# Kernel tuning notes

Measured on AMD Instinct MI355X. Metric: run time of the kernel, lower is better.

The kernel has to match this reference:

```python
import jax, jax.numpy as jnp
from jax import lax
import numpy as np

B, S, H, NF, K, POOL = 64, 1024, 256, 256, 7, 3  # batch, seq, encoded, num_filters, kernel_size, max_pool
C = NF  # input channels must equal num_filters for the per-sample conv


def setup_inputs() -> dict:
    key = jax.random.key(0)
    ks = jax.random.split(key, 8)
    s = lambda k, shape, sc=0.05: jax.random.normal(k, shape, jnp.float32) * sc
    return dict(
        x=jax.random.normal(ks[0], (B, S, C), jnp.float32),
        layer=1,
        gru_kernel_f=s(ks[1], (C, 3 * H)),
        gru_rec_f=s(ks[2], (H, 3 * H)),
        gru_bias_f=jnp.zeros((2, 3 * H), jnp.float32),
        gru_kernel_b=s(ks[3], (C, 3 * H)),
        gru_rec_b=s(ks[4], (H, 3 * H)),
        gru_bias_b=jnp.zeros((2, 3 * H), jnp.float32),
        Wa=s(ks[5], (2 * H, NF * H)),      # hyper_a: Dense(encoded*num_filters), no bias
        Wb=s(ks[6], (H, K * NF)),          # hyper_b: Dense(kernel_size*num_filters), no bias
        conv_bias=jnp.zeros((NF,), jnp.float32),
    )


def _gru_last(x, Wk, Wr, b):
    """Keras GRU (reset_after=True), return final hidden state. x: [B,S,C]."""
    xp = jnp.einsum('bsc,ch->bsh', x, Wk) + b[0]  # precompute input projections
    h0 = jnp.zeros((x.shape[0], Wr.shape[0]), x.dtype)

    def step(h, xt):
        hp = h @ Wr + b[1]
        xz, xr, xh = jnp.split(xt, 3, axis=-1)
        hz, hr, hn = jnp.split(hp, 3, axis=-1)
        z = jax.nn.sigmoid(xz + hz)
        r = jax.nn.sigmoid(xr + hr)
        hh = jnp.tanh(xh + r * hn)
        return z * h + (1.0 - z) * hh, None

    hT, _ = lax.scan(step, h0, jnp.swapaxes(xp, 0, 1))
    return hT


def reference(x, layer, gru_kernel_f, gru_rec_f, gru_bias_f, gru_kernel_b, gru_rec_b,
              gru_bias_b, Wa, Wb, conv_bias):
    if layer == 0:
        pad = (NF - x.shape[2]) // 2
        x = jnp.pad(x, ((0, 0), (0, 0), (pad, pad)))
    # Bidirectional GRU output (return_sequences=False): concat of final fwd/bwd states
    hf = _gru_last(x, gru_kernel_f, gru_rec_f, gru_bias_f)
    hb = _gru_last(x[:, ::-1], gru_kernel_b, gru_rec_b, gru_bias_b)
    c = jnp.concatenate([hf, hb], axis=-1)  # [B, 2H]
    # Hypernetwork: per-sample conv filters
    a = (c @ Wa).reshape(B, NF, H)                          # filters_a: [B, NF, H]
    fb = jnp.einsum('bne,ef->bnf', a, Wb).reshape(B, NF, NF, K)
    filt = fb.transpose(0, 3, 2, 1)                         # [B, K, C_in, C_out] (tf.transpose reversal)

    def conv1(xi, fi):  # xi [S,C], fi [K,C,C]
        return lax.conv_general_dilated(xi[None], fi, (1,), 'SAME',
                                        dimension_numbers=('NWC', 'WIO', 'NWC'))[0]

    y = jax.vmap(conv1)(x, filt) + conv_bias                # [B, S, NF]
    y = jax.nn.relu(y)
    # MaxPooling1D(pool_size=3), stride 3, VALID
    L = (y.shape[1] // POOL) * POOL
    return y[:, :L].reshape(B, L // POOL, POOL, NF).max(axis=2)
```

## Files before the change

kernel.cpp:

```cpp
#include <hip/hip_runtime.h>
#include <cstddef>

typedef unsigned int  uint;
typedef unsigned short ushort_t;
typedef __attribute__((ext_vector_type(8))) short bf16x8;
typedef __attribute__((ext_vector_type(4))) float f32x4;
typedef __attribute__((ext_vector_type(2))) _Float16 h2_t;

__device__ __forceinline__ short f2bs(float x) {
    union { float f; uint u; } v; v.f = x;
    uint r = v.u + 0x7FFF + ((v.u >> 16) & 1);
    return (short)(r >> 16);
}
__device__ __forceinline__ ushort_t f16b(float x) {
    _Float16 h = (_Float16)x; return __builtin_bit_cast(ushort_t, h);
}
__device__ __forceinline__ float h2f(ushort_t u) {
    return (float)__builtin_bit_cast(_Float16, u);
}
__device__ __forceinline__ float fdot2a(uint a, uint b, float c) {
#if __has_builtin(__builtin_amdgcn_fdot2)
    return __builtin_amdgcn_fdot2(__builtin_bit_cast(h2_t, a), __builtin_bit_cast(h2_t, b), c, false);
#else
    h2_t ha = __builtin_bit_cast(h2_t, a), hb = __builtin_bit_cast(h2_t, b);
    return c + (float)ha.x * (float)hb.x + (float)ha.y * (float)hb.y;
#endif
}
__device__ __forceinline__ float fast_sigmoid(float x) {
    float e = __builtin_amdgcn_exp2f(-1.4426950408889634f * x);
    return __builtin_amdgcn_rcpf(1.f + e);
}
__device__ __forceinline__ float fast_tanh(float x) {
    float e = __builtin_amdgcn_exp2f(2.8853900817779268f * x);
    return 1.f - 2.f * __builtin_amdgcn_rcpf(e + 1.f);
}

#define MFMA16(a,b,c) __builtin_amdgcn_mfma_f32_16x16x32_bf16((a),(b),(c),0,0,0)

__global__ void k_prep_x(const float* __restrict__ x, short* __restrict__ xb) {
    int i = (blockIdx.x * 256 + threadIdx.x) * 4;
    float4 v = *(const float4*)&x[i];
    short o[4] = { f2bs(v.x), f2bs(v.y), f2bs(v.z), f2bs(v.w) };
    *(uint2*)&xb[i] = *(uint2*)o;
}
__global__ void k_prep_wk(const float* __restrict__ kf, const float* __restrict__ kb,
                          short* __restrict__ wkt) {
    int n = blockIdx.x, k = threadIdx.x;
    float v = (n < 768) ? kf[k * 768 + n] : kb[k * 768 + (n - 768)];
    wkt[n * 256 + k] = f2bs(v);
}
__global__ void k_prep_wr(const float* __restrict__ wrf, const float* __restrict__ wrb,
                          uint4* __restrict__ wp) {
    int idx = blockIdx.x * 256 + threadIdx.x;
    int dir = idx / 24576, rem = idx % 24576;
    int g = rem / 8192, rem2 = rem % 8192;
    int kc = rem2 / 256, j = rem2 % 256;
    int col = g * 256 + j;
    const float* w = dir ? wrb : wrf;
    uint c[4];
#pragma unroll
    for (int d = 0; d < 4; d++) {
        int k0 = kc * 8 + d * 2;
        uint lo = f16b(w[k0 * 768 + col]);
        uint hi = f16b(w[(k0 + 1) * 768 + col]);
        c[d] = lo | (hi << 16);
    }
    wp[idx] = make_uint4(c[0], c[1], c[2], c[3]);
}
__global__ void k_prep_wb(const float* __restrict__ wb, short* __restrict__ wbt) {
    int kp = blockIdx.x, e = threadIdx.x;
    int n2 = kp & 255, kk = kp >> 8;
    int f = n2 * 7 + kk;
    wbt[kp * 256 + e] = f2bs(wb[e * 1792 + f]);
}

__global__ __launch_bounds__(512) void k_proj(const short* __restrict__ xb,
        const short* __restrict__ wkt, const float* __restrict__ gbf,
        const float* __restrict__ gbb, ushort_t* __restrict__ xp) {
    __shared__ union {
        struct { short A[128 * 40]; short B[128 * 40]; } st;
        ushort_t E[128 * 136];
    } u;
    int bid = blockIdx.x;
    int nt = bid % 12, mt = bid / 12;
    int r0 = mt * 128, n0 = nt * 128;
    int tid = threadIdx.x, lane = tid & 63, wid = tid >> 6;
    int wm = wid & 1, wn = wid >> 1;
    int q = lane >> 4, c = lane & 15;
    f32x4 acc[4][2];
#pragma unroll
    for (int mi = 0; mi < 4; mi++)
#pragma unroll
        for (int ni = 0; ni < 2; ni++) acc[mi][ni] = (f32x4){0.f, 0.f, 0.f, 0.f};
    int si = tid >> 2, sp = tid & 3;
    for (int kt = 0; kt < 8; kt++) {
        int k0 = kt * 32;
        *(uint4*)&u.st.A[si * 40 + sp * 8] = *(const uint4*)&xb[(r0 + si) * 256 + k0 + sp * 8];
        *(uint4*)&u.st.B[si * 40 + sp * 8] = *(const uint4*)&wkt[(n0 + si) * 256 + k0 + sp * 8];
        __syncthreads();
        bf16x8 af[4], bfr[2];
#pragma unroll
        for (int mi = 0; mi < 4; mi++) af[mi] = *(bf16x8*)&u.st.A[(wm * 64 + mi * 16 + c) * 40 + q * 8];
#pragma unroll
        for (int ni = 0; ni < 2; ni++) bfr[ni] = *(bf16x8*)&u.st.B[(wn * 32 + ni * 16 + c) * 40 + q * 8];
#pragma unroll
        for (int mi = 0; mi < 4; mi++)
#pragma unroll
            for (int ni = 0; ni < 2; ni++) acc[mi][ni] = MFMA16(af[mi], bfr[ni], acc[mi][ni]);
        __syncthreads();
    }
#pragma unroll
    for (int ni = 0; ni < 2; ni++) {
        int ng = n0 + wn * 32 + ni * 16 + c;
        bool d1 = ng >= 768; int nb = d1 ? ng - 768 : ng;
        float bias = d1 ? gbb[nb] : gbf[nb];
#pragma unroll
        for (int mi = 0; mi < 4; mi++)
#pragma unroll
            for (int v = 0; v < 4; v++) {
                int rl = wm * 64 + mi * 16 + q * 4 + v;
                u.E[rl * 136 + wn * 32 + ni * 16 + c] = f16b(acc[mi][ni][v] + bias);
            }
    }
    __syncthreads();
    {
        int i = tid >> 2, p = tid & 3;
        int r = r0 + i, b = r >> 10, t = r & 1023;
        int ng = n0 + p * 32;
        const ushort_t* src = &u.E[i * 136 + p * 32];
        ushort_t* dst;
        if (ng < 768) dst = xp + (size_t)(b * 1024 + t) * 768 + ng;
        else          dst = xp + 50331648ull + (size_t)(b * 1024 + (1023 - t)) * 768 + (ng - 768);
#pragma unroll
        for (int v = 0; v < 4; v++) *(uint4*)&dst[v * 8] = *(const uint4*)&src[v * 8];
    }
}

__global__ __launch_bounds__(512, 2) void k_gru(const uint4* __restrict__ wp,
        const ushort_t* __restrict__ xp, const float* __restrict__ gbf,
        const float* __restrict__ gbb, float* __restrict__ cbuf) {
    int wg = blockIdx.x;
    int dir = wg >> 6, b = wg & 63;
    int tid = threadIdx.x;
    int lane = tid & 63, w = tid >> 6;
    int half = lane >> 5;
    int j = w * 32 + (lane & 31);
    const uint4* W = wp + dir * 24576 + half * 4096 + j;
    uint4 wz[16], wr[16], wn[16];
#pragma unroll
    for (int kc = 0; kc < 16; kc++) {
        wz[kc] = W[kc * 256];
        wr[kc] = W[8192 + kc * 256];
        wn[kc] = W[16384 + kc * 256];
    }
    __shared__ uint4 hbuf[2][32];
    const float* bs = (dir ? gbb : gbf) + 768 + j;
    float bz = bs[0], br = bs[256], bn = bs[512];
    const ushort_t* X = xp + ((size_t)dir * 64 + b) * 786432 + j;
    ushort_t uz = X[0], ur = X[256], un = X[512];
    const ushort_t* Xn = X + 768;
    float h = 0.f;
    if (tid < 32) hbuf[0][tid] = (uint4){0, 0, 0, 0};
    __syncthreads();
#pragma unroll 1
    for (int tt = 0; tt < 1024; tt++) {
        const uint4* hb = &hbuf[tt & 1][half * 16];
        ushort_t nz = Xn[0], nr = Xn[256], nn = Xn[512];
        Xn += 768;
        float az = 0.f, ar = 0.f, an = 0.f;
        uint4 c0 = hb[0], c1 = hb[1], c2 = hb[2], c3 = hb[3];
#pragma unroll
        for (int ch = 0; ch < 4; ch++) {
            uint4 n0, n1, n2, n3;
            if (ch < 3) {
                n0 = hb[ch * 4 + 4]; n1 = hb[ch * 4 + 5];
                n2 = hb[ch * 4 + 6]; n3 = hb[ch * 4 + 7];
            }
            int kb = ch * 4;
#define DOT1(hc, kk)                                                              \
            az = fdot2a(hc.x, wz[kk].x, az); ar = fdot2a(hc.x, wr[kk].x, ar);     \
            an = fdot2a(hc.x, wn[kk].x, an);                                      \
            az = fdot2a(hc.y, wz[kk].y, az); ar = fdot2a(hc.y, wr[kk].y, ar);     \
            an = fdot2a(hc.y, wn[kk].y, an);                                      \
            az = fdot2a(hc.z, wz[kk].z, az); ar = fdot2a(hc.z, wr[kk].z, ar);     \
            an = fdot2a(hc.z, wn[kk].z, an);                                      \
            az = fdot2a(hc.w, wz[kk].w, az); ar = fdot2a(hc.w, wr[kk].w, ar);     \
            an = fdot2a(hc.w, wn[kk].w, an);
            DOT1(c0, kb + 0) DOT1(c1, kb + 1) DOT1(c2, kb + 2) DOT1(c3, kb + 3)
#undef DOT1
            __builtin_amdgcn_sched_barrier(0);
            if (ch < 3) { c0 = n0; c1 = n1; c2 = n2; c3 = n3; }
        }
        az += __shfl_xor(az, 32, 64);
        ar += __shfl_xor(ar, 32, 64);
        an += __shfl_xor(an, 32, 64);
        float z = fast_sigmoid(h2f(uz) + az + bz);
        float r = fast_sigmoid(h2f(ur) + ar + br);
        float hh = fast_tanh(h2f(un) + r * (an + bn));
        h = z * h + (1.f - z) * hh;
        uz = nz; ur = nr; un = nn;
        if (half == 0) ((ushort_t*)&hbuf[(tt & 1) ^ 1][0])[j] = f16b(h);
        __syncthreads();
    }
    if (half == 0) cbuf[b * 512 + dir * 256 + j] = h;
}

__global__ __launch_bounds__(256) void k_hyper1(const float* __restrict__ cbuf,
        const float* __restrict__ Wa, short* __restrict__ aout) {
    __shared__ union {
        struct { short A[64 * 40]; short B[128 * 40]; } st;
        ushort_t E[64 * 136];
    } u;
    int nt = blockIdx.x, n0 = nt * 128;
    int tid = threadIdx.x, lane = tid & 63, wid = tid >> 6;
    int q = lane >> 4, c = lane & 15;
    f32x4 acc[4][2];
#pragma unroll
    for (int mi = 0; mi < 4; mi++)
#pragma unroll
        for (int ni = 0; ni < 2; ni++) acc[mi][ni] = (f32x4){0.f, 0.f, 0.f, 0.f};
    for (int kt = 0; kt < 16; kt++) {
        int k0 = kt * 32;
        {
            int i = tid >> 2, p = tid & 3;
            const float* s = &cbuf[i * 512 + k0 + p * 8];
            short tmp[8];
#pragma unroll
            for (int v = 0; v < 8; v++) tmp[v] = f2bs(s[v]);
            *(uint4*)&u.st.A[i * 40 + p * 8] = *(uint4*)tmp;
        }
        {
            int kk = tid >> 3, nn0 = (tid & 7) * 16;
            const float* s = &Wa[(size_t)(k0 + kk) * 65536 + n0 + nn0];
#pragma unroll
            for (int l = 0; l < 16; l++) u.st.B[(nn0 + l) * 40 + kk] = f2bs(s[l]);
        }
        __syncthreads();
        bf16x8 af[4], bfr[2];
#pragma unroll
        for (int mi = 0; mi < 4; mi++) af[mi] = *(bf16x8*)&u.st.A[(mi * 16 + c) * 40 + q * 8];
#pragma unroll
        for (int ni = 0; ni < 2; ni++) bfr[ni] = *(bf16x8*)&u.st.B[(wid * 32 + ni * 16 + c) * 40 + q * 8];
#pragma unroll
        for (int mi = 0; mi < 4; mi++)
#pragma unroll
            for (int ni = 0; ni < 2; ni++) acc[mi][ni] = MFMA16(af[mi], bfr[ni], acc[mi][ni]);
        __syncthreads();
    }
#pragma unroll
    for (int ni = 0; ni < 2; ni++)
#pragma unroll
        for (int mi = 0; mi < 4; mi++)
#pragma unroll
            for (int v = 0; v < 4; v++)
                u.E[(mi * 16 + q * 4 + v) * 136 + wid * 32 + ni * 16 + c] =
                    (ushort_t)f2bs(acc[mi][ni][v]);
    __syncthreads();
    {
        int i = tid >> 2, p = tid & 3;
        short* dst = aout + (size_t)i * 65536 + n0 + p * 32;
        const ushort_t* src = &u.E[i * 136 + p * 32];
#pragma unroll
        for (int v = 0; v < 4; v++) *(uint4*)&dst[v * 8] = *(const uint4*)&src[v * 8];
    }
}

__global__ __launch_bounds__(512) void k_hyper2(const short* __restrict__ a,
        const short* __restrict__ wbt, short* __restrict__ wc) {
    __shared__ union {
        struct { short A[128 * 40]; short B[128 * 40]; } st;
        ushort_t E[128 * 136];
    } u;
    int bid = blockIdx.x;
    int nt = bid % 14, mt = bid / 14;
    int r0 = mt * 128, n0 = nt * 128;
    int tid = threadIdx.x, lane = tid & 63, wid = tid >> 6;
    int wm = wid & 1, wn = wid >> 1;
    int q = lane >> 4, c = lane & 15;
    f32x4 acc[4][2];
#pragma unroll
    for (int mi = 0; mi < 4; mi++)
#pragma unroll
        for (int ni = 0; ni < 2; ni++) acc[mi][ni] = (f32x4){0.f, 0.f, 0.f, 0.f};
    int si = tid >> 2, sp = tid & 3;
    for (int kt = 0; kt < 8; kt++) {
        int k0 = kt * 32;
        *(uint4*)&u.st.A[si * 40 + sp * 8] = *(const uint4*)&a[(r0 + si) * 256 + k0 + sp * 8];
        *(uint4*)&u.st.B[si * 40 + sp * 8] = *(const uint4*)&wbt[(n0 + si) * 256 + k0 + sp * 8];
        __syncthreads();
        bf16x8 af[4], bfr[2];
#pragma unroll
        for (int mi = 0; mi < 4; mi++) af[mi] = *(bf16x8*)&u.st.A[(wm * 64 + mi * 16 + c) * 40 + q * 8];
#pragma unroll
        for (int ni = 0; ni < 2; ni++) bfr[ni] = *(bf16x8*)&u.st.B[(wn * 32 + ni * 16 + c) * 40 + q * 8];
#pragma unroll
        for (int mi = 0; mi < 4; mi++)
#pragma unroll
            for (int ni = 0; ni < 2; ni++) acc[mi][ni] = MFMA16(af[mi], bfr[ni], acc[mi][ni]);
        __syncthreads();
    }
#pragma unroll
    for (int ni = 0; ni < 2; ni++)
#pragma unroll
        for (int mi = 0; mi < 4; mi++)
#pragma unroll
            for (int v = 0; v < 4; v++)
                u.E[(wm * 64 + mi * 16 + q * 4 + v) * 136 + wn * 32 + ni * 16 + c] =
                    (ushort_t)f2bs(acc[mi][ni][v]);
    __syncthreads();
    {
        int i = tid >> 2, p = tid & 3;
        int r = r0 + i, b = r >> 8, co = r & 255;
        short* dst = wc + (size_t)(b * 256 + co) * 1792 + n0 + p * 32;
        const ushort_t* src = &u.E[i * 136 + p * 32];
#pragma unroll
        for (int v = 0; v < 4; v++) *(uint4*)&dst[v * 8] = *(const uint4*)&src[v * 8];
    }
}

__global__ __launch_bounds__(512) void k_conv(const short* __restrict__ xb,
        const short* __restrict__ wc, const float* __restrict__ cbias,
        float* __restrict__ out) {
    __shared__ union {
        struct { short A[128 * 72]; short B[256 * 72]; } st;
        ushort_t Y[128 * 256];
    } u;
    int bid = blockIdx.x;
    int bb = bid & 63, mt = bid >> 6;
    int s0 = mt * 126, p0 = mt * 42;
    int tid = threadIdx.x, lane = tid & 63, wid = tid >> 6;
    int wm = wid & 1, wn = wid >> 1;
    int q = lane >> 4, c = lane & 15;
    const short* xbb = xb + (size_t)bb * 262144;
    const short* wcb = wc + (size_t)bb * 458752;
    f32x4 acc[4][4];
#pragma unroll
    for (int mi = 0; mi < 4; mi++)
#pragma unroll
        for (int ni = 0; ni < 4; ni++) acc[mi][ni] = (f32x4){0.f, 0.f, 0.f, 0.f};
    for (int kc = 0; kc < 28; kc++) {
        int k = kc >> 2, c0 = (kc & 3) * 64;
        {
            int i = tid >> 2, p = tid & 3;
            int rs = s0 + i + k - 3;
            uint4 v0 = {0, 0, 0, 0}, v1 = {0, 0, 0, 0};
            if (rs >= 0 && rs < 1024) {
                const uint4* s = (const uint4*)&xbb[rs * 256 + c0 + p * 16];
                v0 = s[0]; v1 = s[1];
            }
            uint4* d = (uint4*)&u.st.A[i * 72 + p * 16];
            d[0] = v0; d[1] = v1;
        }
        {
            int co = tid >> 1, p = tid & 1;
            const uint4* s = (const uint4*)&wcb[co * 1792 + kc * 64 + p * 32];
            uint4* d = (uint4*)&u.st.B[co * 72 + p * 32];
            d[0] = s[0]; d[1] = s[1]; d[2] = s[2]; d[3] = s[3];
        }
        __syncthreads();
        bf16x8 af[4][2], bfr[4][2];
#pragma unroll
        for (int mi = 0; mi < 4; mi++)
#pragma unroll
            for (int kt = 0; kt < 2; kt++)
                af[mi][kt] = *(bf16x8*)&u.st.A[(wm * 64 + mi * 16 + c) * 72 + kt * 32 + q * 8];
#pragma unroll
        for (int ni = 0; ni < 4; ni++)
#pragma unroll
            for (int kt = 0; kt < 2; kt++)
                bfr[ni][kt] = *(bf16x8*)&u.st.B[(wn * 64 + ni * 16 + c) * 72 + kt * 32 + q * 8];
#pragma unroll
        for (int kt = 0; kt < 2; kt++)
#pragma unroll
            for (int mi = 0; mi < 4; mi++)
#pragma unroll
                for (int ni = 0; ni < 4; ni++)
                    acc[mi][ni] = MFMA16(af[mi][kt], bfr[ni][kt], acc[mi][ni]);
        __syncthreads();
    }
#pragma unroll
    for (int ni = 0; ni < 4; ni++) {
        int cg = wn * 64 + ni * 16 + c;
        float bias = cbias[cg];
#pragma unroll
        for (int mi = 0; mi < 4; mi++)
#pragma unroll
            for (int v = 0; v < 4; v++) {
                int rl = wm * 64 + mi * 16 + q * 4 + v;
                float val = acc[mi][ni][v] + bias;
                u.Y[rl * 256 + cg] = f16b(fmaxf(val, 0.f));
            }
    }
    __syncthreads();
    for (int it = 0; it < 21; it++) {
        int idx = it * 512 + tid;
        int pp = idx >> 8, co = idx & 255;
        int p = p0 + pp;
        if (p < 341) {
            float a0 = h2f(u.Y[(3 * pp) * 256 + co]);
            float a1 = h2f(u.Y[(3 * pp + 1) * 256 + co]);
            float a2 = h2f(u.Y[(3 * pp + 2) * 256 + co]);
            out[(size_t)(bb * 341 + p) * 256 + co] = fmaxf(fmaxf(a0, a1), a2);
        }
    }
}

extern "C" void kernel_launch(void* const* d_in, const int* in_sizes, int n_in,
                              void* d_out, int out_size, void* d_ws, size_t ws_size,
                              hipStream_t stream) {
    const float* x    = (const float*)d_in[0];
    const float* gkf  = (const float*)d_in[2];
    const float* grf  = (const float*)d_in[3];
    const float* gbf  = (const float*)d_in[4];
    const float* gkb  = (const float*)d_in[5];
    const float* grb  = (const float*)d_in[6];
    const float* gbb  = (const float*)d_in[7];
    const float* Wa   = (const float*)d_in[8];
    const float* Wb   = (const float*)d_in[9];
    const float* cbias= (const float*)d_in[10];
    float* out = (float*)d_out;
    char* ws = (char*)d_ws;

    short*    xb   = (short*)(ws);
    ushort_t* xp   = (ushort_t*)(ws + 33554432);
    short*    wkt  = (short*)(ws + 234881024);
    uint4*    wp   = (uint4*)(ws + 235667456);
    short*    wbt  = (short*)(ws + 236453888);
    float*    cbuf = (float*)(ws + 237371392);
    short*    aout = (short*)(ws + 237502464);
    short*    wc   = (short*)(ws + 245891072);

    hipLaunchKernelGGL(k_prep_x,  dim3(16384), dim3(256), 0, stream, x, xb);
    hipLaunchKernelGGL(k_prep_wk, dim3(1536),  dim3(256), 0, stream, gkf, gkb, wkt);
    hipLaunchKernelGGL(k_prep_wr, dim3(192),   dim3(256), 0, stream, grf, grb, wp);
    hipLaunchKernelGGL(k_prep_wb, dim3(1792),  dim3(256), 0, stream, Wb, wbt);
    hipLaunchKernelGGL(k_proj,    dim3(6144),  dim3(512), 0, stream, xb, wkt, gbf, gbb, xp);
    hipLaunchKernelGGL(k_gru,     dim3(128),   dim3(512), 0, stream, wp, xp, gbf, gbb, cbuf);
    hipLaunchKernelGGL(k_hyper1,  dim3(512),   dim3(256), 0, stream, cbuf, Wa, aout);
    hipLaunchKernelGGL(k_hyper2,  dim3(1792),  dim3(512), 0, stream, aout, wbt, wc);
    hipLaunchKernelGGL(k_conv,    dim3(576),   dim3(512), 0, stream, xb, wc, cbias, out);
}
```

Measured before the change: 1.570 ms.

## Repartition GRU recurrent matvec: two columns per lane, K split four ways

The recurrent GRU kernel now has each lane compute two adjacent output columns over a quarter of the hidden dimension, instead of one column over half. Weights are repacked into a per-k-pair uint layout, and hidden-state LDS reads use a rotated per-quarter offset to avoid bank conflicts. Partial sums are reduced with two shuffle stages. The aim is fewer LDS reads of h per FMA and better dot-product throughput on the serial critical path, at the cost of extra shuffles and select logic.

```diff
diff --git a/kernel.cpp b/kernel.cpp
--- a/kernel.cpp
+++ b/kernel.cpp
@@ -50,22 +50,18 @@
     wkt[n * 256 + k] = f2bs(v);
 }
 __global__ void k_prep_wr(const float* __restrict__ wrf, const float* __restrict__ wrb,
-                          uint4* __restrict__ wp) {
+                          uint* __restrict__ wp2) {
     int idx = blockIdx.x * 256 + threadIdx.x;
-    int dir = idx / 24576, rem = idx % 24576;
-    int g = rem / 8192, rem2 = rem % 8192;
-    int kc = rem2 / 256, j = rem2 % 256;
+    int j = idx & 255;
+    int rest = idx >> 8;
+    int p = rest & 127;
+    int gg = rest >> 7;
+    int g = gg % 3, dir = gg / 3;
+    const float* w = dir ? wrb : wrf;
     int col = g * 256 + j;
-    const float* w = dir ? wrb : wrf;
-    uint c[4];
-#pragma unroll
-    for (int d = 0; d < 4; d++) {
-        int k0 = kc * 8 + d * 2;
-        uint lo = f16b(w[k0 * 768 + col]);
-        uint hi = f16b(w[(k0 + 1) * 768 + col]);
-        c[d] = lo | (hi << 16);
-    }
-    wp[idx] = make_uint4(c[0], c[1], c[2], c[3]);
+    uint lo = f16b(w[(2 * p) * 768 + col]);
+    uint hi = f16b(w[(2 * p + 1) * 768 + col]);
+    wp2[idx] = lo | (hi << 16);
 }
 __global__ void k_prep_wb(const float* __restrict__ wb, short* __restrict__ wbt) {
     int kp = blockIdx.x, e = threadIdx.x;
@@ -136,73 +132,109 @@
     }
 }
 
-__global__ __launch_bounds__(512, 2) void k_gru(const uint4* __restrict__ wp,
+__global__ __launch_bounds__(512, 2) void k_gru(const uint* __restrict__ wp2,
         const ushort_t* __restrict__ xp, const float* __restrict__ gbf,
         const float* __restrict__ gbb, float* __restrict__ cbuf) {
     int wg = blockIdx.x;
     int dir = wg >> 6, b = wg & 63;
     int tid = threadIdx.x;
     int lane = tid & 63, w = tid >> 6;
-    int half = lane >> 5;
-    int j = w * 32 + (lane & 31);
-    const uint4* W = wp + dir * 24576 + half * 4096 + j;
-    uint4 wz[16], wr[16], wn[16];
-#pragma unroll
-    for (int kc = 0; kc < 16; kc++) {
-        wz[kc] = W[kc * 256];
-        wr[kc] = W[8192 + kc * 256];
-        wn[kc] = W[16384 + kc * 256];
-    }
-    __shared__ uint4 hbuf[2][32];
-    const float* bs = (dir ? gbb : gbf) + 768 + j;
+    int jl = lane & 15;
+    int kh = (lane >> 4) & 3;
+    int hi = lane >> 5;
+    int j0 = w * 32 + jl * 2;
+    int jsel = j0 + hi;
+
+    const uint* WB = wp2 + dir * 98304;
+    uint2 wreg[3][8][4];
+#pragma unroll
+    for (int g = 0; g < 3; g++)
+#pragma unroll
+        for (int i = 0; i < 8; i++)
+#pragma unroll
+            for (int d = 0; d < 4; d++) {
+                int p = kh * 32 + ((i + kh) & 7) * 4 + d;
+                wreg[g][i][d] = *(const uint2*)&WB[(g * 128 + p) * 256 + j0];
+            }
+
+    __shared__ __align__(16) uint hb[2][128];
+    const float* bs = (dir ? gbb : gbf) + 768 + jsel;
     float bz = bs[0], br = bs[256], bn = bs[512];
-    const ushort_t* X = xp + ((size_t)dir * 64 + b) * 786432 + j;
+    const ushort_t* X = xp + ((size_t)dir * 64 + b) * 786432 + jsel;
     ushort_t uz = X[0], ur = X[256], un = X[512];
     const ushort_t* Xn = X + 768;
     float h = 0.f;
-    if (tid < 32) hbuf[0][tid] = (uint4){0, 0, 0, 0};
+    if (tid < 128) hb[0][tid] = 0u;
     __syncthreads();
+
+    const int off0 = kh * 128 + (((0 + kh) & 7) << 4);
+    const int off1 = kh * 128 + (((1 + kh) & 7) << 4);
+    const int off2 = kh * 128 + (((2 + kh) & 7) << 4);
+    const int off3 = kh * 128 + (((3 + kh) & 7) << 4);
+    const int off4 = kh * 128 + (((4 + kh) & 7) << 4);
+    const int off5 = kh * 128 + (((5 + kh) & 7) << 4);
+    const int off6 = kh * 128 + (((6 + kh) & 7) << 4);
+    const int off7 = kh * 128 + (((7 + kh) & 7) << 4);
+
+#define LDH(off) (*(const uint4*)((const char*)hbp + (off)))
+#define DOT8(cv, ii)                                                                     \
+    a00 = fdot2a(cv.x, wreg[0][ii][0].x, a00); a01 = fdot2a(cv.x, wreg[0][ii][0].y, a01);\
+    a10 = fdot2a(cv.x, wreg[1][ii][0].x, a10); a11 = fdot2a(cv.x, wreg[1][ii][0].y, a11);\
+    a20 = fdot2a(cv.x, wreg[2][ii][0].x, a20); a21 = fdot2a(cv.x, wreg[2][ii][0].y, a21);\
+    a00 = fdot2a(cv.y, wreg[0][ii][1].x, a00); a01 = fdot2a(cv.y, wreg[0][ii][1].y, a01);\
+    a10 = fdot2a(cv.y, wreg[1][ii][1].x, a10); a11 = fdot2a(cv.y, wreg[1][ii][1].y, a11);\
+    a20 = fdot2a(cv.y, wreg[2][ii][1].x, a20); a21 = fdot2a(cv.y, wreg[2][ii][1].y, a21);\
+    a00 = fdot2a(cv.z, wreg[0][ii][2].x, a00); a01 = fdot2a(cv.z, wreg[0][ii][2].y, a01);\
+    a10 = fdot2a(cv.z, wreg[1][ii][2].x, a10); a11 = fdot2a(cv.z, wreg[1][ii][2].y, a11);\
+    a20 = fdot2a(cv.z, wreg[2][ii][2].x, a20); a21 = fdot2a(cv.z, wreg[2][ii][2].y, a21);\
+    a00 = fdot2a(cv.w, wreg[0][ii][3].x, a00); a01 = fdot2a(cv.w, wreg[0][ii][3].y, a01);\
+    a10 = fdot2a(cv.w, wreg[1][ii][3].x, a10); a11 = fdot2a(cv.w, wreg[1][ii][3].y, a11);\
+    a20 = fdot2a(cv.w, wreg[2][ii][3].x, a20); a21 = fdot2a(cv.w, wreg[2][ii][3].y, a21);
+
 #pragma unroll 1
     for (int tt = 0; tt < 1024; tt++) {
-        const uint4* hb = &hbuf[tt & 1][half * 16];
+        const char* hbp = (const char*)&hb[tt & 1][0];
         ushort_t nz = Xn[0], nr = Xn[256], nn = Xn[512];
         Xn += 768;
-        float az = 0.f, ar = 0.f, an = 0.f;
-        uint4 c0 = hb[0], c1 = hb[1], c2 = hb[2], c3 = hb[3];
-#pragma unroll
-        for (int ch = 0; ch < 4; ch++) {
-            uint4 n0, n1, n2, n3;
-            if (ch < 3) {
-                n0 = hb[ch * 4 + 4]; n1 = hb[ch * 4 + 5];
-                n2 = hb[ch * 4 + 6]; n3 = hb[ch * 4 + 7];
-            }
-            int kb = ch * 4;
-#define DOT1(hc, kk)                                                              \
-            az = fdot2a(hc.x, wz[kk].x, az); ar = fdot2a(hc.x, wr[kk].x, ar);     \
-            an = fdot2a(hc.x, wn[kk].x, an);                                      \
-            az = fdot2a(hc.y, wz[kk].y, az); ar = fdot2a(hc.y, wr[kk].y, ar);     \
-            an = fdot2a(hc.y, wn[kk].y, an);                                      \
-            az = fdot2a(hc.z, wz[kk].z, az); ar = fdot2a(hc.z, wr[kk].z, ar);     \
-            an = fdot2a(hc.z, wn[kk].z, an);                                      \
-            az = fdot2a(hc.w, wz[kk].w, az); ar = fdot2a(hc.w, wr[kk].w, ar);     \
-            an = fdot2a(hc.w, wn[kk].w, an);
-            DOT1(c0, kb + 0) DOT1(c1, kb + 1) DOT1(c2, kb + 2) DOT1(c3, kb + 3)
-#undef DOT1
-            __builtin_amdgcn_sched_barrier(0);
-            if (ch < 3) { c0 = n0; c1 = n1; c2 = n2; c3 = n3; }
-        }
-        az += __shfl_xor(az, 32, 64);
-        ar += __shfl_xor(ar, 32, 64);
-        an += __shfl_xor(an, 32, 64);
-        float z = fast_sigmoid(h2f(uz) + az + bz);
-        float r = fast_sigmoid(h2f(ur) + ar + br);
-        float hh = fast_tanh(h2f(un) + r * (an + bn));
+        float a00 = 0.f, a01 = 0.f, a10 = 0.f, a11 = 0.f, a20 = 0.f, a21 = 0.f;
+        uint4 c0 = LDH(off0), c1 = LDH(off1);
+        uint4 n0 = LDH(off2), n1 = LDH(off3);
+        DOT8(c0, 0) DOT8(c1, 1)
+        __builtin_amdgcn_sched_barrier(0);
+        c0 = n0; c1 = n1;
+        n0 = LDH(off4); n1 = LDH(off5);
+        DOT8(c0, 2) DOT8(c1, 3)
+        __builtin_amdgcn_sched_barrier(0);
+        c0 = n0; c1 = n1;
+        n0 = LDH(off6); n1 = LDH(off7);
+        DOT8(c0, 4) DOT8(c1, 5)
+        __builtin_amdgcn_sched_barrier(0);
+        c0 = n0; c1 = n1;
+        DOT8(c0, 6) DOT8(c1, 7)
+
+        float s0, s1;
+        s0 = a00 + __shfl_xor(a00, 32, 64); s1 = a01 + __shfl_xor(a01, 32, 64);
+        float vz = hi ? s1 : s0;
+        s0 = a10 + __shfl_xor(a10, 32, 64); s1 = a11 + __shfl_xor(a11, 32, 64);
+        float vr = hi ? s1 : s0;
+        s0 = a20 + __shfl_xor(a20, 32, 64); s1 = a21 + __shfl_xor(a21, 32, 64);
+        float vn = hi ? s1 : s0;
+        vz += __shfl_xor(vz, 16, 64);
+        vr += __shfl_xor(vr, 16, 64);
+        vn += __shfl_xor(vn, 16, 64);
+
+        float z = fast_sigmoid(h2f(uz) + vz + bz);
+        float r = fast_sigmoid(h2f(ur) + vr + br);
+        float hh = fast_tanh(h2f(un) + r * (vn + bn));
         h = z * h + (1.f - z) * hh;
         uz = nz; ur = nr; un = nn;
-        if (half == 0) ((ushort_t*)&hbuf[(tt & 1) ^ 1][0])[j] = f16b(h);
-        __syncthreads();
-    }
-    if (half == 0) cbuf[b * 512 + dir * 256 + j] = h;
+        if (!(lane & 16))
+            ((ushort_t*)&hb[(tt & 1) ^ 1][0])[w * 32 + jl * 2 + hi] = f16b(h);
+        __syncthreads();
+    }
+#undef DOT8
+#undef LDH
+    if (!(lane & 16)) cbuf[b * 512 + dir * 256 + jsel] = h;
 }
 
 __global__ __launch_bounds__(256) void k_hyper1(const float* __restrict__ cbuf,
@@ -424,7 +456,7 @@
     short*    xb   = (short*)(ws);
     ushort_t* xp   = (ushort_t*)(ws + 33554432);
     short*    wkt  = (short*)(ws + 234881024);
-    uint4*    wp   = (uint4*)(ws + 235667456);
+    uint*     wp2  = (uint*)(ws + 235667456);
     short*    wbt  = (short*)(ws + 236453888);
     float*    cbuf = (float*)(ws + 237371392);
     short*    aout = (short*)(ws + 237502464);
@@ -432,10 +464,10 @@
 
     hipLaunchKernelGGL(k_prep_x,  dim3(16384), dim3(256), 0, stream, x, xb);
     hipLaunchKernelGGL(k_prep_wk, dim3(1536),  dim3(256), 0, stream, gkf, gkb, wkt);
-    hipLaunchKernelGGL(k_prep_wr, dim3(192),   dim3(256), 0, stream, grf, grb, wp);
+    hipLaunchKernelGGL(k_prep_wr, dim3(768),   dim3(256), 0, stream, grf, grb, wp2);
     hipLaunchKernelGGL(k_prep_wb, dim3(1792),  dim3(256), 0, stream, Wb, wbt);
     hipLaunchKernelGGL(k_proj,    dim3(6144),  dim3(512), 0, stream, xb, wkt, gbf, gbb, xp);
-    hipLaunchKernelGGL(k_gru,     dim3(128),   dim3(512), 0, stream, wp, xp, gbf, gbb, cbuf);
+    hipLaunchKernelGGL(k_gru,     dim3(128),   dim3(512), 0, stream, wp2, xp, gbf, gbb, cbuf);
     hipLaunchKernelGGL(k_hyper1,  dim3(512),   dim3(256), 0, stream, cbuf, Wa, aout);
     hipLaunchKernelGGL(k_hyper2,  dim3(1792),  dim3(512), 0, stream, aout, wbt, wc);
     hipLaunchKernelGGL(k_conv,    dim3(576),   dim3(512), 0, stream, xb, wc, cbias, out);
```

Measured after the change: 1.669 ms. +6.3%, slower.

## Batch GRU recurrence over 16 samples per block using f16 MFMA

Applied to the files above, without the earlier changes.

The recurrent GRU step now runs on fp16 MFMA instead of per-lane fdot2 dot products. Each block handles 16 batch samples of one direction, with the recurrent weights held in registers as MFMA B-fragments. The hidden state sits in a swizzled LDS buffer that serves as the A operand. This cuts the launch from 128 blocks to 8 and amortises the weight registers across samples, but uses only 8 CUs for the serial 1024-step loop and adds more per-step gate math per thread.

```diff
diff --git a/kernel.cpp b/kernel.cpp
--- a/kernel.cpp
+++ b/kernel.cpp
@@ -4,6 +4,7 @@
 typedef unsigned int  uint;
 typedef unsigned short ushort_t;
 typedef __attribute__((ext_vector_type(8))) short bf16x8;
+typedef __attribute__((ext_vector_type(8))) _Float16 f16x8;
 typedef __attribute__((ext_vector_type(4))) float f32x4;
 typedef __attribute__((ext_vector_type(2))) _Float16 h2_t;
 
@@ -18,14 +19,6 @@
 __device__ __forceinline__ float h2f(ushort_t u) {
     return (float)__builtin_bit_cast(_Float16, u);
 }
-__device__ __forceinline__ float fdot2a(uint a, uint b, float c) {
-#if __has_builtin(__builtin_amdgcn_fdot2)
-    return __builtin_amdgcn_fdot2(__builtin_bit_cast(h2_t, a), __builtin_bit_cast(h2_t, b), c, false);
-#else
-    h2_t ha = __builtin_bit_cast(h2_t, a), hb = __builtin_bit_cast(h2_t, b);
-    return c + (float)ha.x * (float)hb.x + (float)ha.y * (float)hb.y;
-#endif
-}
 __device__ __forceinline__ float fast_sigmoid(float x) {
     float e = __builtin_amdgcn_exp2f(-1.4426950408889634f * x);
     return __builtin_amdgcn_rcpf(1.f + e);
@@ -36,6 +29,7 @@
 }
 
 #define MFMA16(a,b,c) __builtin_amdgcn_mfma_f32_16x16x32_bf16((a),(b),(c),0,0,0)
+#define MFMAH(a,b,c)  __builtin_amdgcn_mfma_f32_16x16x32_f16((a),(b),(c),0,0,0)
 
 __global__ void k_prep_x(const float* __restrict__ x, short* __restrict__ xb) {
     int i = (blockIdx.x * 256 + threadIdx.x) * 4;
@@ -49,23 +43,11 @@
     float v = (n < 768) ? kf[k * 768 + n] : kb[k * 768 + (n - 768)];
     wkt[n * 256 + k] = f2bs(v);
 }
-__global__ void k_prep_wr(const float* __restrict__ wrf, const float* __restrict__ wrb,
-                          uint4* __restrict__ wp) {
-    int idx = blockIdx.x * 256 + threadIdx.x;
-    int dir = idx / 24576, rem = idx % 24576;
-    int g = rem / 8192, rem2 = rem % 8192;
-    int kc = rem2 / 256, j = rem2 % 256;
-    int col = g * 256 + j;
-    const float* w = dir ? wrb : wrf;
-    uint c[4];
-#pragma unroll
-    for (int d = 0; d < 4; d++) {
-        int k0 = kc * 8 + d * 2;
-        uint lo = f16b(w[k0 * 768 + col]);
-        uint hi = f16b(w[(k0 + 1) * 768 + col]);
-        c[d] = lo | (hi << 16);
-    }
-    wp[idx] = make_uint4(c[0], c[1], c[2], c[3]);
+__global__ void k_prep_wrt(const float* __restrict__ wrf, const float* __restrict__ wrb,
+                           ushort_t* __restrict__ wrt) {
+    int n = blockIdx.x, k = threadIdx.x;
+    float v = (n < 768) ? wrf[k * 768 + n] : wrb[k * 768 + (n - 768)];
+    wrt[n * 256 + k] = f16b(v);
 }
 __global__ void k_prep_wb(const float* __restrict__ wb, short* __restrict__ wbt) {
     int kp = blockIdx.x, e = threadIdx.x;
@@ -136,73 +118,104 @@
     }
 }
 
-__global__ __launch_bounds__(512, 2) void k_gru(const uint4* __restrict__ wp,
+__global__ __launch_bounds__(512, 2) void k_gru(const ushort_t* __restrict__ wrt,
         const ushort_t* __restrict__ xp, const float* __restrict__ gbf,
         const float* __restrict__ gbb, float* __restrict__ cbuf) {
-    int wg = blockIdx.x;
-    int dir = wg >> 6, b = wg & 63;
+    int g = blockIdx.x;
+    int dir = g >> 2;
     int tid = threadIdx.x;
     int lane = tid & 63, w = tid >> 6;
-    int half = lane >> 5;
-    int j = w * 32 + (lane & 31);
-    const uint4* W = wp + dir * 24576 + half * 4096 + j;
-    uint4 wz[16], wr[16], wn[16];
-#pragma unroll
-    for (int kc = 0; kc < 16; kc++) {
-        wz[kc] = W[kc * 256];
-        wr[kc] = W[8192 + kc * 256];
-        wn[kc] = W[16384 + kc * 256];
-    }
-    __shared__ uint4 hbuf[2][32];
-    const float* bs = (dir ? gbb : gbf) + 768 + j;
-    float bz = bs[0], br = bs[256], bn = bs[512];
-    const ushort_t* X = xp + ((size_t)dir * 64 + b) * 786432 + j;
-    ushort_t uz = X[0], ur = X[256], un = X[512];
-    const ushort_t* Xn = X + 768;
-    float h = 0.f;
-    if (tid < 32) hbuf[0][tid] = (uint4){0, 0, 0, 0};
+    int c = lane & 15, q = lane >> 4;
+    int bq = (g & 3) * 16 + q * 4;
+
+    const ushort_t* WD = wrt + (size_t)dir * 196608;
+    f16x8 wfr[6][8];
+#pragma unroll
+    for (int nt = 0; nt < 6; nt++) {
+        int gate = nt >> 1, sub = nt & 1;
+        const ushort_t* wp = WD + (size_t)(gate * 256 + w * 32 + sub * 16 + c) * 256 + q * 8;
+#pragma unroll
+        for (int kt = 0; kt < 8; kt++)
+            wfr[nt][kt] = *(const f16x8*)(wp + kt * 32);
+    }
+
+    const float* bsr = (dir ? gbb : gbf) + 768;
+    float bz[2], br[2], bn[2];
+#pragma unroll
+    for (int sub = 0; sub < 2; sub++) {
+        int j = w * 32 + sub * 16 + c;
+        bz[sub] = bsr[j]; br[sub] = bsr[256 + j]; bn[sub] = bsr[512 + j];
+    }
+
+    const ushort_t* X0 = xp + (size_t)(dir * 64 + bq + 0) * 786432 + w * 32 + c;
+    const ushort_t* X1 = xp + (size_t)(dir * 64 + bq + 1) * 786432 + w * 32 + c;
+    const ushort_t* X2 = xp + (size_t)(dir * 64 + bq + 2) * 786432 + w * 32 + c;
+    const ushort_t* X3 = xp + (size_t)(dir * 64 + bq + 3) * 786432 + w * 32 + c;
+
+    __shared__ ushort_t hbuf[2][16 * 256];
+    {
+        uint4* p = (uint4*)&hbuf[0][0];
+        p[tid] = (uint4){0u, 0u, 0u, 0u};
+    }
     __syncthreads();
+
+    float hreg[2][4];
+#pragma unroll
+    for (int sub = 0; sub < 2; sub++)
+#pragma unroll
+        for (int v = 0; v < 4; v++) hreg[sub][v] = 0.f;
+
+    const int xorm = (lane & 7) << 4;
+
 #pragma unroll 1
     for (int tt = 0; tt < 1024; tt++) {
-        const uint4* hb = &hbuf[tt & 1][half * 16];
-        ushort_t nz = Xn[0], nr = Xn[256], nn = Xn[512];
-        Xn += 768;
-        float az = 0.f, ar = 0.f, an = 0.f;
-        uint4 c0 = hb[0], c1 = hb[1], c2 = hb[2], c3 = hb[3];
-#pragma unroll
-        for (int ch = 0; ch < 4; ch++) {
-            uint4 n0, n1, n2, n3;
-            if (ch < 3) {
-                n0 = hb[ch * 4 + 4]; n1 = hb[ch * 4 + 5];
-                n2 = hb[ch * 4 + 6]; n3 = hb[ch * 4 + 7];
+        ushort_t xv[3][2][4];
+#pragma unroll
+        for (int sub = 0; sub < 2; sub++) {
+            int o = sub * 16;
+            xv[0][sub][0] = X0[o]; xv[1][sub][0] = X0[256 + o]; xv[2][sub][0] = X0[512 + o];
+            xv[0][sub][1] = X1[o]; xv[1][sub][1] = X1[256 + o]; xv[2][sub][1] = X1[512 + o];
+            xv[0][sub][2] = X2[o]; xv[1][sub][2] = X2[256 + o]; xv[2][sub][2] = X2[512 + o];
+            xv[0][sub][3] = X3[o]; xv[1][sub][3] = X3[256 + o]; xv[2][sub][3] = X3[512 + o];
+        }
+        X0 += 768; X1 += 768; X2 += 768; X3 += 768;
+
+        const char* hbp = (const char*)&hbuf[tt & 1][0] + (lane & 15) * 512;
+        f32x4 acc[6];
+#pragma unroll
+        for (int nt = 0; nt < 6; nt++) acc[nt] = (f32x4){0.f, 0.f, 0.f, 0.f};
+#pragma unroll
+        for (int kt = 0; kt < 8; kt++) {
+            f16x8 af = *(const f16x8*)(hbp + ((kt * 64 + q * 16) ^ xorm));
+#pragma unroll
+            for (int nt = 0; nt < 6; nt++) acc[nt] = MFMAH(af, wfr[nt][kt], acc[nt]);
+        }
+
+        char* wb = (char*)&hbuf[(tt & 1) ^ 1][0];
+#pragma unroll
+        for (int sub = 0; sub < 2; sub++)
+#pragma unroll
+            for (int v = 0; v < 4; v++) {
+                float z  = fast_sigmoid(h2f(xv[0][sub][v]) + acc[sub][v]     + bz[sub]);
+                float r  = fast_sigmoid(h2f(xv[1][sub][v]) + acc[2 + sub][v] + br[sub]);
+                float hh = fast_tanh   (h2f(xv[2][sub][v]) + r * (acc[4 + sub][v] + bn[sub]));
+                float hn = z * hreg[sub][v] + (1.f - z) * hh;
+                hreg[sub][v] = hn;
+                int mw = q * 4 + v;
+                int jb = (w * 32 + sub * 16 + c) * 2;
+                *(ushort_t*)(wb + mw * 512 + (jb ^ ((mw & 7) << 4))) = f16b(hn);
             }
-            int kb = ch * 4;
-#define DOT1(hc, kk)                                                              \
-            az = fdot2a(hc.x, wz[kk].x, az); ar = fdot2a(hc.x, wr[kk].x, ar);     \
-            an = fdot2a(hc.x, wn[kk].x, an);                                      \
-            az = fdot2a(hc.y, wz[kk].y, az); ar = fdot2a(hc.y, wr[kk].y, ar);     \
-            an = fdot2a(hc.y, wn[kk].y, an);                                      \
-            az = fdot2a(hc.z, wz[kk].z, az); ar = fdot2a(hc.z, wr[kk].z, ar);     \
-            an = fdot2a(hc.z, wn[kk].z, an);                                      \
-            az = fdot2a(hc.w, wz[kk].w, az); ar = fdot2a(hc.w, wr[kk].w, ar);     \
-            an = fdot2a(hc.w, wn[kk].w, an);
-            DOT1(c0, kb + 0) DOT1(c1, kb + 1) DOT1(c2, kb + 2) DOT1(c3, kb + 3)
-#undef DOT1
-            __builtin_amdgcn_sched_barrier(0);
-            if (ch < 3) { c0 = n0; c1 = n1; c2 = n2; c3 = n3; }
-        }
-        az += __shfl_xor(az, 32, 64);
-        ar += __shfl_xor(ar, 32, 64);
-        an += __shfl_xor(an, 32, 64);
-        float z = fast_sigmoid(h2f(uz) + az + bz);
-        float r = fast_sigmoid(h2f(ur) + ar + br);
-        float hh = fast_tanh(h2f(un) + r * (an + bn));
-        h = z * h + (1.f - z) * hh;
-        uz = nz; ur = nr; un = nn;
-        if (half == 0) ((ushort_t*)&hbuf[(tt & 1) ^ 1][0])[j] = f16b(h);
-        __syncthreads();
-    }
-    if (half == 0) cbuf[b * 512 + dir * 256 + j] = h;
+        __syncthreads();
+    }
+
+#pragma unroll
+    for (int sub = 0; sub < 2; sub++)
+#pragma unroll
+        for (int v = 0; v < 4; v++) {
+            int b = bq + v;
+            int j = w * 32 + sub * 16 + c;
+            cbuf[b * 512 + dir * 256 + j] = hreg[sub][v];
+        }
 }
 
 __global__ __launch_bounds__(256) void k_hyper1(const float* __restrict__ cbuf,
@@ -424,19 +437,19 @@
     short*    xb   = (short*)(ws);
     ushort_t* xp   = (ushort_t*)(ws + 33554432);
     short*    wkt  = (short*)(ws + 234881024);
-    uint4*    wp   = (uint4*)(ws + 235667456);
+    ushort_t* wrt  = (ushort_t*)(ws + 235667456);
     short*    wbt  = (short*)(ws + 236453888);
     float*    cbuf = (float*)(ws + 237371392);
     short*    aout = (short*)(ws + 237502464);
     short*    wc   = (short*)(ws + 245891072);
 
-    hipLaunchKernelGGL(k_prep_x,  dim3(16384), dim3(256), 0, stream, x, xb);
-    hipLaunchKernelGGL(k_prep_wk, dim3(1536),  dim3(256), 0, stream, gkf, gkb, wkt);
-    hipLaunchKernelGGL(k_prep_wr, dim3(192),   dim3(256), 0, stream, grf, grb, wp);
-    hipLaunchKernelGGL(k_prep_wb, dim3(1792),  dim3(256), 0, stream, Wb, wbt);
-    hipLaunchKernelGGL(k_proj,    dim3(6144),  dim3(512), 0, stream, xb, wkt, gbf, gbb, xp);
-    hipLaunchKernelGGL(k_gru,     dim3(128),   dim3(512), 0, stream, wp, xp, gbf, gbb, cbuf);
-    hipLaunchKernelGGL(k_hyper1,  dim3(512),   dim3(256), 0, stream, cbuf, Wa, aout);
-    hipLaunchKernelGGL(k_hyper2,  dim3(1792),  dim3(512), 0, stream, aout, wbt, wc);
-    hipLaunchKernelGGL(k_conv,    dim3(576),   dim3(512), 0, stream, xb, wc, cbias, out);
-}
+    hipLaunchKernelGGL(k_prep_x,   dim3(16384), dim3(256), 0, stream, x, xb);
+    hipLaunchKernelGGL(k_prep_wk,  dim3(1536),  dim3(256), 0, stream, gkf, gkb, wkt);
+    hipLaunchKernelGGL(k_prep_wrt, dim3(1536),  dim3(256), 0, stream, grf, grb, wrt);
+    hipLaunchKernelGGL(k_prep_wb,  dim3(1792),  dim3(256), 0, stream, Wb, wbt);
+    hipLaunchKernelGGL(k_proj,     dim3(6144),  dim3(512), 0, stream, xb, wkt, gbf, gbb, xp);
+    hipLaunchKernelGGL(k_gru,      dim3(8),     dim3(512), 0, stream, wrt, xp, gbf, gbb, cbuf);
+    hipLaunchKernelGGL(k_hyper1,   dim3(512),   dim3(256), 0, stream, cbuf, Wa, aout);
+    hipLaunchKernelGGL(k_hyper2,   dim3(1792),  dim3(512), 0, stream, aout, wbt, wc);
+    hipLaunchKernelGGL(k_conv,     dim3(576),   dim3(512), 0, stream, xb, wc, cbias, out);
+}
```

New measurement: 4.621 ms. 2.94x slower.
